# Kernel optimization log

Hardware: AMD Instinct MI355X
Metric: run time of the kernel (lower is better)

The kernel has to match this reference:

```python
import jax, jax.numpy as jnp
import numpy as np

WS = 7       # window_size
SHIFT = 3    # shift_size
HEADS = 3
EPS = 1e-5


def _rel_index():
    # (2, N) coords of a WS x WS window, then pairwise relative offsets -> flat table index
    coords = np.stack(np.meshgrid(np.arange(WS), np.arange(WS), indexing='ij')).reshape(2, -1)
    rel = (coords[:, :, None] - coords[:, None, :]).transpose(1, 2, 0) + (WS - 1)  # (N,N,2)
    return jnp.asarray(rel[..., 0] * (2 * WS - 1) + rel[..., 1])  # (N,N) int


def _layernorm(x, g, b):
    mu = jnp.mean(x, axis=-1, keepdims=True)
    var = jnp.mean(jnp.square(x - mu), axis=-1, keepdims=True)
    return (x - mu) * jax.lax.rsqrt(var + EPS) * g + b


def setup_inputs() -> dict:
    key = jax.random.key(0)
    ks = jax.random.split(key, 6)
    C, HID = 96, 384
    s = 0.02
    return {
        'x': jax.random.normal(ks[0], (8, C, 224, 224), jnp.float32),
        'norm1_g': jnp.ones((C,), jnp.float32),
        'norm1_b': jnp.zeros((C,), jnp.float32),
        'qkv_w': jax.random.normal(ks[1], (C, 3 * C), jnp.float32) * s,
        'qkv_b': jnp.zeros((3 * C,), jnp.float32),
        'proj_w': jax.random.normal(ks[2], (C, C), jnp.float32) * s,
        'proj_b': jnp.zeros((C,), jnp.float32),
        'rel_bias_table': jax.random.normal(ks[3], ((2 * WS - 1) ** 2, HEADS), jnp.float32) * s,
        'norm2_g': jnp.ones((C,), jnp.float32),
        'norm2_b': jnp.zeros((C,), jnp.float32),
        'fc1_w': jax.random.normal(ks[4], (C, HID), jnp.float32) * s,
        'fc1_b': jnp.zeros((HID,), jnp.float32),
        'fc2_w': jax.random.normal(ks[5], (HID, C), jnp.float32) * s,
        'fc2_b': jnp.zeros((C,), jnp.float32),
    }


def reference(x, norm1_g, norm1_b, qkv_w, qkv_b, proj_w, proj_b,
              rel_bias_table, norm2_g, norm2_b, fc1_w, fc1_b, fc2_w, fc2_b):
    B, C, H, W = x.shape
    N = WS * WS
    dh = C // HEADS

    # norm1 over channels (tokens = flattened spatial)
    xt = x.reshape(B, C, H * W).transpose(0, 2, 1)          # (B, L, C)
    xn = _layernorm(xt, norm1_g, norm1_b)
    xs = xn.transpose(0, 2, 1).reshape(B, C, H, W)
    # H, W divisible by WS -> pad is a no-op; cyclic shift
    xs = jnp.roll(xs, (-SHIFT, -SHIFT), axis=(2, 3))

    # window partition -> (B*nW, N, C)
    xw = xs.reshape(B, C, H // WS, WS, W // WS, WS)
    xw = xw.transpose(0, 2, 4, 3, 5, 1).reshape(-1, N, C)

    # window attention with relative position bias (no shift mask, per source)
    Bw = xw.shape[0]
    qkv = (xw @ qkv_w + qkv_b).reshape(Bw, N, 3, HEADS, dh).transpose(2, 0, 3, 1, 4)
    q, k, v = qkv[0], qkv[1], qkv[2]                        # (Bw, h, N, dh)
    attn = jnp.einsum('bhnd,bhmd->bhnm', q, k) * (dh ** -0.5)
    bias = rel_bias_table[_rel_index().reshape(-1)].reshape(N, N, HEADS).transpose(2, 0, 1)
    attn = jax.nn.softmax(attn + bias, axis=-1)
    out = jnp.einsum('bhnm,bhmd->bhnd', attn, v).transpose(0, 2, 1, 3).reshape(Bw, N, C)
    out = out @ proj_w + proj_b

    # window reverse + unshift
    xr = out.reshape(B, H // WS, W // WS, WS, WS, C)
    xr = xr.transpose(0, 5, 1, 3, 2, 4).reshape(B, C, H, W)
    xr = jnp.roll(xr, (SHIFT, SHIFT), axis=(2, 3))

    x = x + xr                                              # residual 1

    # MLP branch with norm2 (exact GELU, matching torch nn.GELU default)
    xt = x.reshape(B, C, H * W).transpose(0, 2, 1)
    xn = _layernorm(xt, norm2_g, norm2_b)
    h = jax.nn.gelu(xn @ fc1_w + fc1_b, approximate=False)
    h = h @ fc2_w + fc2_b
    return x + h.transpose(0, 2, 1).reshape(B, C, H, W)
```

## Files before the change

### kernel.cpp

```cpp
#include <hip/hip_runtime.h>
#include <hip/hip_bf16.h>
#include <math.h>

#define WSZ 7
#define NTOK 49
#define CH 96
#define HIMG 224
#define WIMG 224
#define HWIMG (224*224)
#define SHIFT_ 3
#define HID 384

typedef __attribute__((ext_vector_type(8))) short bf16x8;
typedef __attribute__((ext_vector_type(4))) float f32x4;
typedef unsigned int u32;
typedef unsigned short u16;

__device__ __forceinline__ u32 pk2(float a, float b) {
    u16 ua = __builtin_bit_cast(u16, __float2bfloat16(a));
    u16 ub = __builtin_bit_cast(u16, __float2bfloat16(b));
    return (u32)ua | ((u32)ub << 16);
}

union FragU { u32 w[4]; bf16x8 v; };

__device__ __forceinline__ bf16x8 regroup(u32 t0w0, u32 t0w1, u32 t1w0, u32 t1w1, int lane) {
    int sl0 = (lane & 15) + ((lane & 16) << 1);
    int sl1 = sl0 + 16;
    u32 x0 = (u32)__shfl((int)t0w0, sl0);
    u32 y0 = (u32)__shfl((int)t1w0, sl0);
    u32 x1 = (u32)__shfl((int)t0w1, sl0);
    u32 y1 = (u32)__shfl((int)t1w1, sl0);
    u32 x2 = (u32)__shfl((int)t0w0, sl1);
    u32 y2 = (u32)__shfl((int)t1w0, sl1);
    u32 x3 = (u32)__shfl((int)t0w1, sl1);
    u32 y3 = (u32)__shfl((int)t1w1, sl1);
    bool lo = lane < 32;
    FragU f;
    f.w[0] = lo ? x0 : y0;
    f.w[1] = lo ? x1 : y1;
    f.w[2] = lo ? x2 : y2;
    f.w[3] = lo ? x3 : y3;
    return f.v;
}

__device__ __forceinline__ float gelu_f(float x) {
    float x2 = x * x;
    float s  = x * (0.7978845608028654f + 0.03567740813636141f * x2);
    float e  = __expf(2.0f * s);
    float th = 1.0f - 2.0f / (e + 1.0f);
    return 0.5f * x * (1.0f + th);
}

__global__ __launch_bounds__(256) void prep_kernel(
    const float* __restrict__ w1, const float* __restrict__ w2,
    const float* __restrict__ pw, const float* __restrict__ qw,
    __hip_bfloat16* __restrict__ ws, int n)
{
    int i = blockIdx.x * 256 + threadIdx.x;
    if (i >= n) return;
    float val = 0.f;
    if (i < 81920) {
        int ch = i / 20480, r = i - ch * 20480;
        int half = r / 10240;
        int rr = r - half * 10240;
        if (rr < 9984) {
            int row = rr / 104, col = rr - row * 104;
            if (col < 96)
                val = (half == 0) ? w1[col * HID + ch * 96 + row]
                                  : w2[(size_t)(ch * 96 + col) * CH + row];
        }
    } else if (i < 92160) {
        int r = i - 81920;
        if (r < 9984) {
            int row = r / 104, col = r - row * 104;
            if (col < 96) val = pw[col * CH + row];
        }
    } else {
        int j = i - 92160;
        int hh = j / 9984, rr = j - hh * 9984;
        int dp = rr / 104, c = rr - dp * 104;
        if (c < 96) {
            int colW = (dp < 32) ? (hh * 32 + dp)
                     : (dp < 64) ? (96 + hh * 32 + dp - 32)
                                 : (192 + hh * 32 + dp - 64);
            val = qw[c * 288 + colW];
        }
    }
    ws[i] = __float2bfloat16(val);
}

__global__ __launch_bounds__(256) void attn2_kernel(
    const float* __restrict__ x,
    const float* __restrict__ g1, const float* __restrict__ b1,
    const __hip_bfloat16* __restrict__ wsW,
    const float* __restrict__ qkv_b, const float* __restrict__ pb,
    const float* __restrict__ btab,
    __hip_bfloat16* __restrict__ projout)
{
    const int tid  = threadIdx.x;
    const int lane = tid & 63;
    const int wv   = tid >> 6;
    const int l15  = lane & 15;
    const int g    = lane >> 4;
    const int bi   = blockIdx.x;
    const int b    = bi >> 8;
    const int wh   = (bi >> 3) & 31;
    const int ww0  = (bi & 7) * 4;
    const int ww   = ww0 + wv;

    __shared__ float btabL[507];
    __shared__ __align__(16) char uniA[43008];

    __hip_bfloat16 (*xsb)[7][32] = (__hip_bfloat16(*)[7][32])uniA;
    __hip_bfloat16 (*vT)[72] = (__hip_bfloat16(*)[72])(uniA + wv * 4608);
    u32* prS = (u32*)(uniA + wv * 4608);

    for (int idx = tid; idx < 507; idx += 256) btabL[idx] = btab[idx];

    const int colBase = ww0 * 7 + 3;
    const int cA  = colBase & ~3;
    const int cb4 = cA >> 2;
    const int a0  = colBase & 3;
    #pragma unroll
    for (int k = 0; k < 21; ++k) {
        int idx = tid + 256 * k;
        int c = idx / 56, rem = idx - c * 56;
        int r = rem >> 3, cf = rem & 7;
        int gr = wh * 7 + 3 + r; if (gr >= HIMG) gr -= HIMG;
        int g4 = cb4 + cf; if (g4 >= 56) g4 -= 56;
        float4 v = *(const float4*)(x + ((size_t)(b * CH + c) * HIMG + gr) * WIMG + g4 * 4);
        uint2 pk;
        pk.x = pk2(v.x, v.y);
        pk.y = pk2(v.z, v.w);
        *(uint2*)&xsb[c][r][cf * 4] = pk;
    }
    __syncthreads();

    bf16x8 xB[4][3];
    #pragma unroll
    for (int it = 0; it < 4; ++it) {
        int i = it * 16 + l15;
        bool real = i < NTOK;
        int yi = i / 7, xi = i - yi * 7;
        int sc = a0 + wv * 7 + xi;
        float raw[24];
        float s0 = 0.f, s1 = 0.f;
        #pragma unroll
        for (int ks = 0; ks < 3; ++ks)
            #pragma unroll
            for (int t = 0; t < 8; ++t) {
                int c = ks * 32 + g * 8 + t;
                float v = real ? __bfloat162float(xsb[c][yi][sc]) : 0.f;
                raw[ks * 8 + t] = v; s0 += v; s1 += v * v;
            }
        s0 += __shfl_xor(s0, 16); s0 += __shfl_xor(s0, 32);
        s1 += __shfl_xor(s1, 16); s1 += __shfl_xor(s1, 32);
        float mu = s0 * (1.0f / CH);
        float rstd = rsqrtf(s1 * (1.0f / CH) - mu * mu + 1e-5f);
        #pragma unroll
        for (int ks = 0; ks < 3; ++ks)
            #pragma unroll
            for (int t = 0; t < 8; ++t) {
                int c = ks * 32 + g * 8 + t;
                float xv = real ? ((raw[ks * 8 + t] - mu) * rstd * g1[c] + b1[c]) : 0.f;
                xB[it][ks][t] = (short)__builtin_bit_cast(u16, __float2bfloat16(xv));
            }
    }
    __syncthreads();

    const float scale = 0.17677669529663687f;
    bf16x8 aoB[3][4];

    for (int h = 0; h < 3; ++h) {
        const __hip_bfloat16* qkvTg = wsW + 92160 + h * 9984;

        float qb[2][4], kb[2][4], vb[2][4];
        #pragma unroll
        for (int dt = 0; dt < 2; ++dt)
            #pragma unroll
            for (int r = 0; r < 4; ++r) {
                int d = h * 32 + dt * 16 + g * 4 + r;
                qb[dt][r] = qkv_b[d];
                kb[dt][r] = qkv_b[96 + d];
                vb[dt][r] = qkv_b[192 + d];
            }

        u32 Qpk[2][4][2];
        #pragma unroll
        for (int dt = 0; dt < 2; ++dt) {
            const __hip_bfloat16* wr = qkvTg + (dt * 16 + l15) * 104 + g * 8;
            bf16x8 a0f = *(const bf16x8*)(wr);
            bf16x8 a1f = *(const bf16x8*)(wr + 32);
            bf16x8 a2f = *(const bf16x8*)(wr + 64);
            #pragma unroll
            for (int it = 0; it < 4; ++it) {
                f32x4 c4 = {0.f, 0.f, 0.f, 0.f};
                c4 = __builtin_amdgcn_mfma_f32_16x16x32_bf16(a0f, xB[it][0], c4, 0, 0, 0);
                c4 = __builtin_amdgcn_mfma_f32_16x16x32_bf16(a1f, xB[it][1], c4, 0, 0, 0);
                c4 = __builtin_amdgcn_mfma_f32_16x16x32_bf16(a2f, xB[it][2], c4, 0, 0, 0);
                Qpk[dt][it][0] = pk2(c4[0] + qb[dt][0], c4[1] + qb[dt][1]);
                Qpk[dt][it][1] = pk2(c4[2] + qb[dt][2], c4[3] + qb[dt][3]);
            }
        }
        bf16x8 QB[4];
        #pragma unroll
        for (int it = 0; it < 4; ++it)
            QB[it] = regroup(Qpk[0][it][0], Qpk[0][it][1], Qpk[1][it][0], Qpk[1][it][1], lane);

        u32 Kpk[2][4][2];
        #pragma unroll
        for (int dt = 0; dt < 2; ++dt) {
            const __hip_bfloat16* wr = qkvTg + (32 + dt * 16 + l15) * 104 + g * 8;
            bf16x8 a0f = *(const bf16x8*)(wr);
            bf16x8 a1f = *(const bf16x8*)(wr + 32);
            bf16x8 a2f = *(const bf16x8*)(wr + 64);
            #pragma unroll
            for (int it = 0; it < 4; ++it) {
                f32x4 c4 = {0.f, 0.f, 0.f, 0.f};
                c4 = __builtin_amdgcn_mfma_f32_16x16x32_bf16(a0f, xB[it][0], c4, 0, 0, 0);
                c4 = __builtin_amdgcn_mfma_f32_16x16x32_bf16(a1f, xB[it][1], c4, 0, 0, 0);
                c4 = __builtin_amdgcn_mfma_f32_16x16x32_bf16(a2f, xB[it][2], c4, 0, 0, 0);
                Kpk[dt][it][0] = pk2(c4[0] + kb[dt][0], c4[1] + kb[dt][1]);
                Kpk[dt][it][1] = pk2(c4[2] + kb[dt][2], c4[3] + kb[dt][3]);
            }
        }
        bf16x8 KA[4];
        #pragma unroll
        for (int it = 0; it < 4; ++it)
            KA[it] = regroup(Kpk[0][it][0], Kpk[0][it][1], Kpk[1][it][0], Kpk[1][it][1], lane);

        #pragma unroll
        for (int dt = 0; dt < 2; ++dt) {
            const __hip_bfloat16* wr = qkvTg + (64 + dt * 16 + l15) * 104 + g * 8;
            bf16x8 a0f = *(const bf16x8*)(wr);
            bf16x8 a1f = *(const bf16x8*)(wr + 32);
            bf16x8 a2f = *(const bf16x8*)(wr + 64);
            #pragma unroll
            for (int it = 0; it < 4; ++it) {
                f32x4 c4 = {0.f, 0.f, 0.f, 0.f};
                c4 = __builtin_amdgcn_mfma_f32_16x16x32_bf16(a0f, xB[it][0], c4, 0, 0, 0);
                c4 = __builtin_amdgcn_mfma_f32_16x16x32_bf16(a1f, xB[it][1], c4, 0, 0, 0);
                c4 = __builtin_amdgcn_mfma_f32_16x16x32_bf16(a2f, xB[it][2], c4, 0, 0, 0);
                #pragma unroll
                for (int r = 0; r < 4; ++r)
                    vT[dt * 16 + g * 4 + r][it * 16 + l15] = __float2bfloat16(c4[r] + vb[dt][r]);
            }
        }
        bf16x8 VBf[2][2];
        #pragma unroll
        for (int dt = 0; dt < 2; ++dt)
            #pragma unroll
            for (int ks = 0; ks < 2; ++ks)
                VBf[dt][ks] = *(const bf16x8*)&vT[dt * 16 + l15][ks * 32 + g * 8];

        #pragma unroll
        for (int it = 0; it < 4; ++it) {
            f32x4 SC[4];
            #pragma unroll
            for (int jt = 0; jt < 4; ++jt) {
                f32x4 z = {0.f, 0.f, 0.f, 0.f};
                SC[jt] = __builtin_amdgcn_mfma_f32_16x16x32_bf16(KA[jt], QB[it], z, 0, 0, 0);
            }
            int i = it * 16 + l15;
            int yi = i / 7, xi = i - yi * 7;
            float p[16];
            float m = -1e30f;
            #pragma unroll
            for (int jt = 0; jt < 4; ++jt)
                #pragma unroll
                for (int r = 0; r < 4; ++r) {
                    int j = jt * 16 + g * 4 + r;
                    int yj = j / 7, xj = j - yj * 7;
                    int rel = (yi - yj + 6) * 13 + (xi - xj + 6);
                    rel = rel < 0 ? 0 : (rel > 168 ? 168 : rel);
                    float s = (j < NTOK) ? (SC[jt][r] * scale + btabL[rel * 3 + h]) : -1e30f;
                    p[jt * 4 + r] = s;
                    m = fmaxf(m, s);
                }
            m = fmaxf(m, __shfl_xor(m, 16));
            m = fmaxf(m, __shfl_xor(m, 32));
            float sum = 0.f;
            #pragma unroll
            for (int q = 0; q < 16; ++q) { float e = __expf(p[q] - m); p[q] = e; sum += e; }
            sum += __shfl_xor(sum, 16);
            sum += __shfl_xor(sum, 32);
            float inv = 1.f / sum;
            u32 Ppk[4][2];
            #pragma unroll
            for (int jt = 0; jt < 4; ++jt) {
                Ppk[jt][0] = pk2(p[jt * 4 + 0] * inv, p[jt * 4 + 1] * inv);
                Ppk[jt][1] = pk2(p[jt * 4 + 2] * inv, p[jt * 4 + 3] * inv);
            }
            bf16x8 PA0 = regroup(Ppk[0][0], Ppk[0][1], Ppk[1][0], Ppk[1][1], lane);
            bf16x8 PA1 = regroup(Ppk[2][0], Ppk[2][1], Ppk[3][0], Ppk[3][1], lane);
            u32 opk[2][2];
            #pragma unroll
            for (int dt = 0; dt < 2; ++dt) {
                f32x4 o = {0.f, 0.f, 0.f, 0.f};
                o = __builtin_amdgcn_mfma_f32_16x16x32_bf16(PA0, VBf[dt][0], o, 0, 0, 0);
                o = __builtin_amdgcn_mfma_f32_16x16x32_bf16(PA1, VBf[dt][1], o, 0, 0, 0);
                opk[dt][0] = pk2(o[0], o[1]);
                opk[dt][1] = pk2(o[2], o[3]);
            }
            aoB[h][it] = regroup(opk[0][0], opk[0][1], opk[1][0], opk[1][1], lane);
        }
    }

    const __hip_bfloat16* pwTg = wsW + 81920;
    for (int it = 0; it < 4; ++it) {
        #pragma unroll
        for (int mt = 0; mt < 6; ++mt) {
            const __hip_bfloat16* wr = pwTg + (mt * 16 + l15) * 104 + g * 8;
            f32x4 cp = {0.f, 0.f, 0.f, 0.f};
            #pragma unroll
            for (int ks = 0; ks < 3; ++ks) {
                bf16x8 af = *(const bf16x8*)(wr + ks * 32);
                cp = __builtin_amdgcn_mfma_f32_16x16x32_bf16(af, aoB[ks][it], cp, 0, 0, 0);
            }
            float v0 = cp[0] + pb[mt * 16 + g * 4 + 0];
            float v1 = cp[1] + pb[mt * 16 + g * 4 + 1];
            float v2 = cp[2] + pb[mt * 16 + g * 4 + 2];
            float v3 = cp[3] + pb[mt * 16 + g * 4 + 3];
            prS[l15 * 52 + mt * 8 + g * 2 + 0] = pk2(v0, v1);
            prS[l15 * 52 + mt * 8 + g * 2 + 1] = pk2(v2, v3);
        }
        #pragma unroll
        for (int s = 0; s < 3; ++s) {
            int chunk = lane + 64 * s;
            int row = chunk / 12, q = chunk - row * 12;
            int tok = it * 16 + row;
            if (tok < NTOK) {
                int yi = tok / 7, xi = tok - yi * 7;
                int hh = wh * 7 + yi + SHIFT_; if (hh >= HIMG) hh -= HIMG;
                int wp = ww * 7 + xi + SHIFT_; if (wp >= WIMG) wp -= WIMG;
                float4 val = *(const float4*)((const char*)prS + row * 208 + q * 16);
                *(float4*)(projout + ((size_t)b * HWIMG + hh * WIMG + wp) * 96 + q * 8) = val;
            }
        }
    }
}

__global__ __launch_bounds__(512, 4) void mlp2_kernel(
    const float* __restrict__ x, const __hip_bfloat16* __restrict__ projout,
    const float* __restrict__ g2, const float* __restrict__ b2,
    const float* __restrict__ bb1, const float* __restrict__ bb2,
    const __hip_bfloat16* __restrict__ wsW,
    float* __restrict__ out)
{
    const int tid = threadIdx.x;
    const int lane = tid & 63, wv = tid >> 6;
    const int l15 = lane & 15, g = lane >> 4;
    const int b = blockIdx.x / 392;
    const int hw0 = (blockIdx.x % 392) * 128;
    const int m0 = wv * 16;
    const int t = tid & 127;
    const int c0 = tid >> 7;

    __shared__ __align__(16) char WREG[46592];
    __shared__ __align__(16) __hip_bfloat16 xnS[128][104];
    __shared__ float part0[4][128], part1[4][128];
    __shared__ float muS[128], rsS[128];
    __shared__ float bb1S[HID];

    __hip_bfloat16 (*w1T)[104]  = (__hip_bfloat16(*)[104])WREG;
    __hip_bfloat16 (*w2T)[104]  = (__hip_bfloat16(*)[104])(WREG + 20480);
    __hip_bfloat16 (*obuf)[104] = (__hip_bfloat16(*)[104])WREG;

    float xreg[24];

    for (int idx = tid, k = 0; idx < 96 * 128; idx += 512, ++k) {
        int c = idx >> 7, tt = idx & 127;
        xreg[k] = x[(size_t)(b * CH + c) * HWIMG + hw0 + tt];
    }
    #pragma unroll
    for (int s = 0; s < 3; ++s) {
        int chunk = tid + 512 * s;
        int row = chunk / 12, q = chunk - row * 12;
        *(float4*)&xnS[row][q * 8] =
            *(const float4*)(projout + ((size_t)b * HWIMG + hw0 + row) * 96 + q * 8);
    }
    for (int idx = tid; idx < HID; idx += 512) bb1S[idx] = bb1[idx];
    __syncthreads();

    {
        float s0 = 0.f, s1 = 0.f;
        #pragma unroll
        for (int k = 0; k < 24; ++k) {
            int c = c0 + 4 * k;
            float v = xreg[k] + __bfloat162float(xnS[t][c]);
            xreg[k] = v; s0 += v; s1 += v * v;
        }
        part0[c0][t] = s0; part1[c0][t] = s1;
    }
    __syncthreads();
    if (tid < 128) {
        float s0 = part0[0][tid] + part0[1][tid] + part0[2][tid] + part0[3][tid];
        float s1 = part1[0][tid] + part1[1][tid] + part1[2][tid] + part1[3][tid];
        float m = s0 * (1.0f / CH);
        muS[tid] = m;
        rsS[tid] = rsqrtf(s1 * (1.0f / CH) - m * m + 1e-5f);
    }
    __syncthreads();
    #pragma unroll
    for (int k = 0; k < 24; ++k) {
        int c = c0 + 4 * k;
        xnS[t][c] = __float2bfloat16((xreg[k] - muS[t]) * rsS[t] * g2[c] + b2[c]);
    }
    __syncthreads();

    bf16x8 xbf[3];
    #pragma unroll
    for (int ks = 0; ks < 3; ++ks)
        xbf[ks] = *(const bf16x8*)&xnS[m0 + l15][ks * 32 + g * 8];

    f32x4 acc[6];
    #pragma unroll
    for (int mt = 0; mt < 6; ++mt)
        #pragma unroll
        for (int r = 0; r < 4; ++r)
            acc[mt][r] = bb2[mt * 16 + g * 4 + r];

    for (int ch = 0; ch < 4; ++ch) {
        {
            const float4* src = (const float4*)wsW + (size_t)ch * 2560;
            float4* dst = (float4*)WREG;
            #pragma unroll
            for (int i = tid; i < 2560; i += 512) dst[i] = src[i];
        }
        __syncthreads();

        u32 hpk[6][2];
        #pragma unroll
        for (int mt = 0; mt < 6; ++mt) {
            f32x4 f = {0.f, 0.f, 0.f, 0.f};
            #pragma unroll
            for (int ks = 0; ks < 3; ++ks) {
                bf16x8 af = *(const bf16x8*)&w1T[mt * 16 + l15][ks * 32 + g * 8];
                f = __builtin_amdgcn_mfma_f32_16x16x32_bf16(af, xbf[ks], f, 0, 0, 0);
            }
            float gl[4];
            #pragma unroll
            for (int r = 0; r < 4; ++r) {
                float a = f[r] + bb1S[ch * 96 + mt * 16 + g * 4 + r];
                gl[r] = gelu_f(a);
            }
            hpk[mt][0] = pk2(gl[0], gl[1]);
            hpk[mt][1] = pk2(gl[2], gl[3]);
        }
        bf16x8 hf[3];
        hf[0] = regroup(hpk[0][0], hpk[0][1], hpk[1][0], hpk[1][1], lane);
        hf[1] = regroup(hpk[2][0], hpk[2][1], hpk[3][0], hpk[3][1], lane);
        hf[2] = regroup(hpk[4][0], hpk[4][1], hpk[5][0], hpk[5][1], lane);

        #pragma unroll
        for (int mt = 0; mt < 6; ++mt) {
            #pragma unroll
            for (int ks = 0; ks < 3; ++ks) {
                bf16x8 af = *(const bf16x8*)&w2T[mt * 16 + l15][ks * 32 + g * 8];
                acc[mt] = __builtin_amdgcn_mfma_f32_16x16x32_bf16(af, hf[ks], acc[mt], 0, 0, 0);
            }
        }
        __syncthreads();
    }

    #pragma unroll
    for (int mt = 0; mt < 6; ++mt)
        #pragma unroll
        for (int r = 0; r < 4; ++r)
            obuf[m0 + l15][mt * 16 + g * 4 + r] = __float2bfloat16(acc[mt][r]);
    __syncthreads();
    #pragma unroll
    for (int k = 0; k < 24; ++k) {
        int c = c0 + 4 * k;
        out[(size_t)(b * CH + c) * HWIMG + hw0 + t] = xreg[k] + __bfloat162float(obuf[t][c]);
    }
}

__global__ __launch_bounds__(256) void attn_mfma_kernel(
    const float* __restrict__ x,
    const float* __restrict__ g1, const float* __restrict__ b1,
    const float* __restrict__ qkv_w, const float* __restrict__ qkv_b,
    const float* __restrict__ btab,
    float* __restrict__ ao)
{
    const int tid  = threadIdx.x;
    const int lane = tid & 63;
    const int wv   = tid >> 6;
    const int l15  = lane & 15;
    const int g    = lane >> 4;
    const int wid  = blockIdx.x * 4 + wv;
    const int b    = wid >> 10;
    const int wh   = (wid >> 5) & 31;
    const int ww   = wid & 31;

    __shared__ __align__(16) __hip_bfloat16 wT[96][104];
    __shared__ float btabL[507];
    __shared__ __align__(16) __hip_bfloat16 vT[4][32][72];
    __shared__ __align__(16) __hip_bfloat16 Ob[4][64][36];

    int to_h = 0, to_w = 0;
    if (lane < NTOK) {
        int yl = lane / 7, xl = lane - yl * 7;
        to_h = wh * 7 + yl + SHIFT_; if (to_h >= HIMG) to_h -= HIMG;
        to_w = ww * 7 + xl + SHIFT_; if (to_w >= WIMG) to_w -= WIMG;
    }

    bf16x8 xB[4][3];
    #pragma unroll
    for (int it = 0; it < 4; ++it) {
        int i = it * 16 + l15;
        bool real = i < NTOK;
        int yi = i / 7, xi = i - yi * 7;
        int hh = wh * 7 + yi + SHIFT_; if (hh >= HIMG) hh -= HIMG;
        int wp = ww * 7 + xi + SHIFT_; if (wp >= WIMG) wp -= WIMG;
        float raw[24];
        float s0 = 0.f, s1 = 0.f;
        #pragma unroll
        for (int ks = 0; ks < 3; ++ks)
            #pragma unroll
            for (int t = 0; t < 8; ++t) {
                int c = ks * 32 + g * 8 + t;
                float v = real ? x[((size_t)(b * CH + c) * HIMG + hh) * WIMG + wp] : 0.f;
                raw[ks * 8 + t] = v; s0 += v; s1 += v * v;
            }
        s0 += __shfl_xor(s0, 16); s0 += __shfl_xor(s0, 32);
        s1 += __shfl_xor(s1, 16); s1 += __shfl_xor(s1, 32);
        float mu = s0 * (1.0f / CH);
        float rstd = rsqrtf(s1 * (1.0f / CH) - mu * mu + 1e-5f);
        #pragma unroll
        for (int ks = 0; ks < 3; ++ks)
            #pragma unroll
            for (int t = 0; t < 8; ++t) {
                int c = ks * 32 + g * 8 + t;
                float xv = real ? ((raw[ks * 8 + t] - mu) * rstd * g1[c] + b1[c]) : 0.f;
                xB[it][ks][t] = (short)__builtin_bit_cast(u16, __float2bfloat16(xv));
            }
    }

    const float scale = 0.17677669529663687f;

    for (int h = 0; h < 3; ++h) {
        __syncthreads();
        for (int idx = tid; idx < 96 * 96; idx += 256) {
            int c = idx / 96, dp = idx - c * 96;
            int col = (dp < 32) ? (h * 32 + dp) : (dp < 64) ? (96 + h * 32 + dp - 32)
                                                            : (192 + h * 32 + dp - 64);
            wT[dp][c] = __float2bfloat16(qkv_w[c * 288 + col]);
        }
        if (h == 0)
            for (int idx = tid; idx < 507; idx += 256) btabL[idx] = btab[idx];
        __syncthreads();

        float qb[2][4], kb[2][4], vb[2][4];
        #pragma unroll
        for (int dt = 0; dt < 2; ++dt)
            #pragma unroll
            for (int r = 0; r < 4; ++r) {
                int d = h * 32 + dt * 16 + g * 4 + r;
                qb[dt][r] = qkv_b[d];
                kb[dt][r] = qkv_b[96 + d];
                vb[dt][r] = qkv_b[192 + d];
            }

        u32 Qpk[2][4][2];
        #pragma unroll
        for (int dt = 0; dt < 2; ++dt) {
            bf16x8 a0 = *(const bf16x8*)&wT[dt * 16 + l15][0 * 32 + g * 8];
            bf16x8 a1 = *(const bf16x8*)&wT[dt * 16 + l15][1 * 32 + g * 8];
            bf16x8 a2 = *(const bf16x8*)&wT[dt * 16 + l15][2 * 32 + g * 8];
            #pragma unroll
            for (int it = 0; it < 4; ++it) {
                f32x4 c4 = {0.f, 0.f, 0.f, 0.f};
                c4 = __builtin_amdgcn_mfma_f32_16x16x32_bf16(a0, xB[it][0], c4, 0, 0, 0);
                c4 = __builtin_amdgcn_mfma_f32_16x16x32_bf16(a1, xB[it][1], c4, 0, 0, 0);
                c4 = __builtin_amdgcn_mfma_f32_16x16x32_bf16(a2, xB[it][2], c4, 0, 0, 0);
                Qpk[dt][it][0] = pk2(c4[0] + qb[dt][0], c4[1] + qb[dt][1]);
                Qpk[dt][it][1] = pk2(c4[2] + qb[dt][2], c4[3] + qb[dt][3]);
            }
        }
        bf16x8 QB[4];
        #pragma unroll
        for (int it = 0; it < 4; ++it)
            QB[it] = regroup(Qpk[0][it][0], Qpk[0][it][1], Qpk[1][it][0], Qpk[1][it][1], lane);

        u32 Kpk[2][4][2];
        #pragma unroll
        for (int dt = 0; dt < 2; ++dt) {
            bf16x8 a0 = *(const bf16x8*)&wT[32 + dt * 16 + l15][0 * 32 + g * 8];
            bf16x8 a1 = *(const bf16x8*)&wT[32 + dt * 16 + l15][1 * 32 + g * 8];
            bf16x8 a2 = *(const bf16x8*)&wT[32 + dt * 16 + l15][2 * 32 + g * 8];
            #pragma unroll
            for (int it = 0; it < 4; ++it) {
                f32x4 c4 = {0.f, 0.f, 0.f, 0.f};
                c4 = __builtin_amdgcn_mfma_f32_16x16x32_bf16(a0, xB[it][0], c4, 0, 0, 0);
                c4 = __builtin_amdgcn_mfma_f32_16x16x32_bf16(a1, xB[it][1], c4, 0, 0, 0);
                c4 = __builtin_amdgcn_mfma_f32_16x16x32_bf16(a2, xB[it][2], c4, 0, 0, 0);
                Kpk[dt][it][0] = pk2(c4[0] + kb[dt][0], c4[1] + kb[dt][1]);
                Kpk[dt][it][1] = pk2(c4[2] + kb[dt][2], c4[3] + kb[dt][3]);
            }
        }
        bf16x8 KA[4];
        #pragma unroll
        for (int it = 0; it < 4; ++it)
            KA[it] = regroup(Kpk[0][it][0], Kpk[0][it][1], Kpk[1][it][0], Kpk[1][it][1], lane);

        #pragma unroll
        for (int dt = 0; dt < 2; ++dt) {
            bf16x8 a0 = *(const bf16x8*)&wT[64 + dt * 16 + l15][0 * 32 + g * 8];
            bf16x8 a1 = *(const bf16x8*)&wT[64 + dt * 16 + l15][1 * 32 + g * 8];
            bf16x8 a2 = *(const bf16x8*)&wT[64 + dt * 16 + l15][2 * 32 + g * 8];
            #pragma unroll
            for (int it = 0; it < 4; ++it) {
                f32x4 c4 = {0.f, 0.f, 0.f, 0.f};
                c4 = __builtin_amdgcn_mfma_f32_16x16x32_bf16(a0, xB[it][0], c4, 0, 0, 0);
                c4 = __builtin_amdgcn_mfma_f32_16x16x32_bf16(a1, xB[it][1], c4, 0, 0, 0);
                c4 = __builtin_amdgcn_mfma_f32_16x16x32_bf16(a2, xB[it][2], c4, 0, 0, 0);
                #pragma unroll
                for (int r = 0; r < 4; ++r)
                    vT[wv][dt * 16 + g * 4 + r][it * 16 + l15] = __float2bfloat16(c4[r] + vb[dt][r]);
            }
        }
        bf16x8 VBf[2][2];
        #pragma unroll
        for (int dt = 0; dt < 2; ++dt)
            #pragma unroll
            for (int ks = 0; ks < 2; ++ks)
                VBf[dt][ks] = *(const bf16x8*)&vT[wv][dt * 16 + l15][ks * 32 + g * 8];

        #pragma unroll
        for (int it = 0; it < 4; ++it) {
            f32x4 SC[4];
            #pragma unroll
            for (int jt = 0; jt < 4; ++jt) {
                f32x4 z = {0.f, 0.f, 0.f, 0.f};
                SC[jt] = __builtin_amdgcn_mfma_f32_16x16x32_bf16(KA[jt], QB[it], z, 0, 0, 0);
            }
            int i = it * 16 + l15;
            int yi = i / 7, xi = i - yi * 7;
            float p[16];
            float m = -1e30f;
            #pragma unroll
            for (int jt = 0; jt < 4; ++jt)
                #pragma unroll
                for (int r = 0; r < 4; ++r) {
                    int j = jt * 16 + g * 4 + r;
                    int yj = j / 7, xj = j - yj * 7;
                    int rel = (yi - yj + 6) * 13 + (xi - xj + 6);
                    rel = rel < 0 ? 0 : (rel > 168 ? 168 : rel);
                    float s = (j < NTOK) ? (SC[jt][r] * scale + btabL[rel * 3 + h]) : -1e30f;
                    p[jt * 4 + r] = s;
                    m = fmaxf(m, s);
                }
            m = fmaxf(m, __shfl_xor(m, 16));
            m = fmaxf(m, __shfl_xor(m, 32));
            float sum = 0.f;
            #pragma unroll
            for (int q = 0; q < 16; ++q) { float e = __expf(p[q] - m); p[q] = e; sum += e; }
            sum += __shfl_xor(sum, 16);
            sum += __shfl_xor(sum, 32);
            float inv = 1.f / sum;
            u32 Ppk[4][2];
            #pragma unroll
            for (int jt = 0; jt < 4; ++jt) {
                Ppk[jt][0] = pk2(p[jt * 4 + 0] * inv, p[jt * 4 + 1] * inv);
                Ppk[jt][1] = pk2(p[jt * 4 + 2] * inv, p[jt * 4 + 3] * inv);
            }
            bf16x8 PA0 = regroup(Ppk[0][0], Ppk[0][1], Ppk[1][0], Ppk[1][1], lane);
            bf16x8 PA1 = regroup(Ppk[2][0], Ppk[2][1], Ppk[3][0], Ppk[3][1], lane);
            #pragma unroll
            for (int dt = 0; dt < 2; ++dt) {
                f32x4 o = {0.f, 0.f, 0.f, 0.f};
                o = __builtin_amdgcn_mfma_f32_16x16x32_bf16(PA0, VBf[dt][0], o, 0, 0, 0);
                o = __builtin_amdgcn_mfma_f32_16x16x32_bf16(PA1, VBf[dt][1], o, 0, 0, 0);
                #pragma unroll
                for (int r = 0; r < 4; ++r)
                    Ob[wv][it * 16 + g * 4 + r][dt * 16 + l15] = __float2bfloat16(o[r]);
            }
        }

        if (lane < NTOK) {
            #pragma unroll 8
            for (int ch = 0; ch < 32; ++ch)
                ao[((size_t)(b * CH + h * 32 + ch) * HIMG + to_h) * WIMG + to_w] =
                    __bfloat162float(Ob[wv][lane][ch]);
        }
    }
}

__global__ __launch_bounds__(512, 4) void fuse2_kernel(
    const float* __restrict__ x, const float* ao,
    const float* __restrict__ pw, const float* __restrict__ pb,
    const float* __restrict__ g2, const float* __restrict__ b2,
    const float* __restrict__ w1, const float* __restrict__ bb1,
    const float* __restrict__ w2, const float* __restrict__ bb2,
    const __hip_bfloat16* __restrict__ wsW, int useWs,
    float* out)
{
    const int tid = threadIdx.x;
    const int lane = tid & 63, wv = tid >> 6;
    const int l15 = lane & 15, g = lane >> 4;
    const int b = blockIdx.x / 392;
    const int hw0 = (blockIdx.x % 392) * 128;
    const int m0 = wv * 16;
    const int t = tid & 127;
    const int c0 = tid >> 7;

    __shared__ __align__(16) char WREG[46592];
    __shared__ __align__(16) __hip_bfloat16 xnS[128][104];
    __shared__ float part0[4][128], part1[4][128];
    __shared__ float muS[128], rsS[128];
    __shared__ float bb1S[HID];

    __hip_bfloat16 (*pwT)[104]   = (__hip_bfloat16(*)[104])WREG;
    __hip_bfloat16 (*projS)[104] = (__hip_bfloat16(*)[104])(WREG + 19968);
    __hip_bfloat16 (*w1T)[104]   = (__hip_bfloat16(*)[104])WREG;
    __hip_bfloat16 (*w2T)[104]   = (__hip_bfloat16(*)[104])(WREG + 20480);
    __hip_bfloat16 (*obuf)[104]  = (__hip_bfloat16(*)[104])WREG;

    float xreg[24];

    for (int idx = tid, k = 0; idx < 96 * 128; idx += 512, ++k) {
        int c = idx >> 7, tt = idx & 127;
        size_t gi = (size_t)(b * CH + c) * HWIMG + hw0 + tt;
        xreg[k] = x[gi];
        xnS[tt][c] = __float2bfloat16(ao[gi]);
    }
    if (useWs) {
        const float4* src = (const float4*)wsW + 10240;
        float4* dst = (float4*)WREG;
        for (int i = tid; i < 1280; i += 512) dst[i] = src[i];
    } else {
        for (int idx = tid; idx < 96 * 96; idx += 512) {
            int c = idx / 96, oc = idx - c * 96;
            pwT[oc][c] = __float2bfloat16(pw[c * 96 + oc]);
        }
    }
    for (int idx = tid; idx < HID; idx += 512) bb1S[idx] = bb1[idx];
    __syncthreads();

    {
        bf16x8 bfr[3];
        #pragma unroll
        for (int ks = 0; ks < 3; ++ks)
            bfr[ks] = *(const bf16x8*)&xnS[m0 + l15][ks * 32 + g * 8];
        #pragma unroll
        for (int mt = 0; mt < 6; ++mt) {
            f32x4 cp = {0.f, 0.f, 0.f, 0.f};
            #pragma unroll
            for (int ks = 0; ks < 3; ++ks) {
                bf16x8 af = *(const bf16x8*)&pwT[mt * 16 + l15][ks * 32 + g * 8];
                cp = __builtin_amdgcn_mfma_f32_16x16x32_bf16(af, bfr[ks], cp, 0, 0, 0);
            }
            #pragma unroll
            for (int r = 0; r < 4; ++r) {
                int oc = mt * 16 + g * 4 + r;
                projS[m0 + l15][oc] = __float2bfloat16(cp[r] + pb[oc]);
            }
        }
    }
    __syncthreads();

    {
        float s0 = 0.f, s1 = 0.f;
        #pragma unroll
        for (int k = 0; k < 24; ++k) {
            int c = c0 + 4 * k;
            float v = xreg[k] + __bfloat162float(projS[t][c]);
            xreg[k] = v; s0 += v; s1 += v * v;
        }
        part0[c0][t] = s0; part1[c0][t] = s1;
    }
    __syncthreads();
    if (tid < 128) {
        float s0 = part0[0][tid] + part0[1][tid] + part0[2][tid] + part0[3][tid];
        float s1 = part1[0][tid] + part1[1][tid] + part1[2][tid] + part1[3][tid];
        float m = s0 * (1.0f / CH);
        muS[tid] = m;
        rsS[tid] = rsqrtf(s1 * (1.0f / CH) - m * m + 1e-5f);
    }
    __syncthreads();
    #pragma unroll
    for (int k = 0; k < 24; ++k) {
        int c = c0 + 4 * k;
        xnS[t][c] = __float2bfloat16((xreg[k] - muS[t]) * rsS[t] * g2[c] + b2[c]);
    }
    __syncthreads();

    bf16x8 xbf[3];
    #pragma unroll
    for (int ks = 0; ks < 3; ++ks)
        xbf[ks] = *(const bf16x8*)&xnS[m0 + l15][ks * 32 + g * 8];

    f32x4 acc[6];
    #pragma unroll
    for (int mt = 0; mt < 6; ++mt)
        #pragma unroll
        for (int r = 0; r < 4; ++r)
            acc[mt][r] = bb2[mt * 16 + g * 4 + r];

    for (int ch = 0; ch < 4; ++ch) {
        if (useWs) {
            const float4* src = (const float4*)wsW + (size_t)ch * 2560;
            float4* dst = (float4*)WREG;
            #pragma unroll
            for (int i = tid; i < 2560; i += 512) dst[i] = src[i];
        } else {
            for (int idx = tid; idx < 2 * 96 * 96; idx += 512) {
                if (idx < 9216) {
                    int kk = idx / 96, n = idx - kk * 96;
                    w1T[n][kk] = __float2bfloat16(w1[kk * HID + ch * 96 + n]);
                } else {
                    int j = idx - 9216;
                    int kk = j / 96, n = j - kk * 96;
                    w2T[n][kk] = __float2bfloat16(w2[(size_t)(ch * 96 + kk) * CH + n]);
                }
            }
        }
        __syncthreads();

        u32 hpk[6][2];
        #pragma unroll
        for (int mt = 0; mt < 6; ++mt) {
            f32x4 f = {0.f, 0.f, 0.f, 0.f};
            #pragma unroll
            for (int ks = 0; ks < 3; ++ks) {
                bf16x8 af = *(const bf16x8*)&w1T[mt * 16 + l15][ks * 32 + g * 8];
                f = __builtin_amdgcn_mfma_f32_16x16x32_bf16(af, xbf[ks], f, 0, 0, 0);
            }
            float gl[4];
            #pragma unroll
            for (int r = 0; r < 4; ++r) {
                float a = f[r] + bb1S[ch * 96 + mt * 16 + g * 4 + r];
                gl[r] = gelu_f(a);
            }
            hpk[mt][0] = pk2(gl[0], gl[1]);
            hpk[mt][1] = pk2(gl[2], gl[3]);
        }
        bf16x8 hf[3];
        hf[0] = regroup(hpk[0][0], hpk[0][1], hpk[1][0], hpk[1][1], lane);
        hf[1] = regroup(hpk[2][0], hpk[2][1], hpk[3][0], hpk[3][1], lane);
        hf[2] = regroup(hpk[4][0], hpk[4][1], hpk[5][0], hpk[5][1], lane);

        #pragma unroll
        for (int mt = 0; mt < 6; ++mt)
            #pragma unroll
            for (int ks = 0; ks < 3; ++ks) {
                bf16x8 af = *(const bf16x8*)&w2T[mt * 16 + l15][ks * 32 + g * 8];
                acc[mt] = __builtin_amdgcn_mfma_f32_16x16x32_bf16(af, hf[ks], acc[mt], 0, 0, 0);
            }
        __syncthreads();
    }

    #pragma unroll
    for (int mt = 0; mt < 6; ++mt)
        #pragma unroll
        for (int r = 0; r < 4; ++r)
            obuf[m0 + l15][mt * 16 + g * 4 + r] = __float2bfloat16(acc[mt][r]);
    __syncthreads();
    #pragma unroll
    for (int k = 0; k < 24; ++k) {
        int c = c0 + 4 * k;
        out[(size_t)(b * CH + c) * HWIMG + hw0 + t] = xreg[k] + __bfloat162float(obuf[t][c]);
    }
}

extern "C" void kernel_launch(void* const* d_in, const int* in_sizes, int n_in,
                              void* d_out, int out_size, void* d_ws, size_t ws_size,
                              hipStream_t stream) {
    const float* x    = (const float*)d_in[0];
    const float* n1g  = (const float*)d_in[1];
    const float* n1b  = (const float*)d_in[2];
    const float* qkvw = (const float*)d_in[3];
    const float* qkvb = (const float*)d_in[4];
    const float* pw   = (const float*)d_in[5];
    const float* pbv  = (const float*)d_in[6];
    const float* bt   = (const float*)d_in[7];
    const float* n2g  = (const float*)d_in[8];
    const float* n2b  = (const float*)d_in[9];
    const float* f1w  = (const float*)d_in[10];
    const float* f1b  = (const float*)d_in[11];
    const float* f2w  = (const float*)d_in[12];
    const float* f2b  = (const float*)d_in[13];
    float* out = (float*)d_out;

    const size_t FULL_NEED = 262144ull + 77070336ull;
    if (ws_size >= FULL_NEED) {
        __hip_bfloat16* wsW = (__hip_bfloat16*)d_ws;
        __hip_bfloat16* projout = (__hip_bfloat16*)((char*)d_ws + 262144);
        prep_kernel<<<477, 256, 0, stream>>>(f1w, f2w, pw, qkvw, wsW, 122112);
        attn2_kernel<<<2048, 256, 0, stream>>>(x, n1g, n1b, wsW, qkvb, pbv, bt, projout);
        mlp2_kernel<<<3136, 512, 0, stream>>>(x, projout, n2g, n2b, f1b, f2b, wsW, out);
    } else {
        int useWs = (ws_size >= 184320) ? 1 : 0;
        if (useWs)
            prep_kernel<<<360, 256, 0, stream>>>(f1w, f2w, pw, qkvw, (__hip_bfloat16*)d_ws, 92160);
        attn_mfma_kernel<<<2048, 256, 0, stream>>>(x, n1g, n1b, qkvw, qkvb, bt, out);
        fuse2_kernel<<<3136, 512, 0, stream>>>(x, out, pw, pbv, n2g, n2b, f1w, f1b, f2w, f2b,
                                               (const __hip_bfloat16*)d_ws, useWs, out);
    }
}
```

Baseline: 455.4 us.

## Shrink MLP kernel LDS via per-wave LayerNorm and single weight buffer

The MLP kernel now computes residual-add and LayerNorm per token inside each wave using MFMA fragment layout and cross-lane shuffles, which removes the partial-sum shared arrays and several block barriers. Weight staging now uses one half-size LDS buffer that is reloaded between fc1 and fc2 for each hidden chunk, so shared memory drops from about 74KB to about 28KB, allowing more blocks per CU. In exchange it adds two extra barriers and a second global weight load per chunk. The global reads and writes of x become strided per lane rather than coalesced across tokens.

```diff
diff --git a/kernel.cpp b/kernel.cpp
--- a/kernel.cpp
+++ b/kernel.cpp
@@ -21,6 +21,7 @@
     u16 ub = __builtin_bit_cast(u16, __float2bfloat16(b));
     return (u32)ua | ((u32)ub << 16);
 }
+__device__ __forceinline__ float bflo(u32 u) { return __builtin_bit_cast(float, u << 16); }
 
 union FragU { u32 w[4]; bf16x8 v; };
 
@@ -353,26 +354,15 @@
     const int l15 = lane & 15, g = lane >> 4;
     const int b = blockIdx.x / 392;
     const int hw0 = (blockIdx.x % 392) * 128;
-    const int m0 = wv * 16;
-    const int t = tid & 127;
-    const int c0 = tid >> 7;
-
-    __shared__ __align__(16) char WREG[46592];
-    __shared__ __align__(16) __hip_bfloat16 xnS[128][104];
-    __shared__ float part0[4][128], part1[4][128];
-    __shared__ float muS[128], rsS[128];
+    const int tok = wv * 16 + l15;
+
+    __shared__ __align__(16) char SB[26624];
     __shared__ float bb1S[HID];
 
-    __hip_bfloat16 (*w1T)[104]  = (__hip_bfloat16(*)[104])WREG;
-    __hip_bfloat16 (*w2T)[104]  = (__hip_bfloat16(*)[104])(WREG + 20480);
-    __hip_bfloat16 (*obuf)[104] = (__hip_bfloat16(*)[104])WREG;
-
-    float xreg[24];
-
-    for (int idx = tid, k = 0; idx < 96 * 128; idx += 512, ++k) {
-        int c = idx >> 7, tt = idx & 127;
-        xreg[k] = x[(size_t)(b * CH + c) * HWIMG + hw0 + tt];
-    }
+    __hip_bfloat16 (*xnS)[104]  = (__hip_bfloat16(*)[104])SB;
+    __hip_bfloat16 (*wT)[104]   = (__hip_bfloat16(*)[104])SB;
+    __hip_bfloat16 (*obuf)[104] = (__hip_bfloat16(*)[104])SB;
+
     #pragma unroll
     for (int s = 0; s < 3; ++s) {
         int chunk = tid + 512 * s;
@@ -383,50 +373,55 @@
     for (int idx = tid; idx < HID; idx += 512) bb1S[idx] = bb1[idx];
     __syncthreads();
 
-    {
-        float s0 = 0.f, s1 = 0.f;
-        #pragma unroll
-        for (int k = 0; k < 24; ++k) {
-            int c = c0 + 4 * k;
-            float v = xreg[k] + __bfloat162float(xnS[t][c]);
-            xreg[k] = v; s0 += v; s1 += v * v;
-        }
-        part0[c0][t] = s0; part1[c0][t] = s1;
-    }
-    __syncthreads();
-    if (tid < 128) {
-        float s0 = part0[0][tid] + part0[1][tid] + part0[2][tid] + part0[3][tid];
-        float s1 = part1[0][tid] + part1[1][tid] + part1[2][tid] + part1[3][tid];
-        float m = s0 * (1.0f / CH);
-        muS[tid] = m;
-        rsS[tid] = rsqrtf(s1 * (1.0f / CH) - m * m + 1e-5f);
-    }
-    __syncthreads();
-    #pragma unroll
-    for (int k = 0; k < 24; ++k) {
-        int c = c0 + 4 * k;
-        xnS[t][c] = __float2bfloat16((xreg[k] - muS[t]) * rsS[t] * g2[c] + b2[c]);
-    }
-    __syncthreads();
+    float xr[24];
+    float s0 = 0.f, s1 = 0.f;
+    bf16x8 pf[3];
+    #pragma unroll
+    for (int ks = 0; ks < 3; ++ks)
+        pf[ks] = *(const bf16x8*)&xnS[tok][ks * 32 + g * 8];
+    const float* xb = x + (size_t)(b * CH) * HWIMG + hw0 + tok;
+    #pragma unroll
+    for (int ks = 0; ks < 3; ++ks)
+        #pragma unroll
+        for (int j = 0; j < 8; ++j) {
+            int c = ks * 32 + g * 8 + j;
+            float xv = xb[(size_t)c * HWIMG];
+            float v = xv + bflo((u32)(u16)pf[ks][j]);
+            xr[ks * 8 + j] = v; s0 += v; s1 += v * v;
+        }
+    s0 += __shfl_xor(s0, 16); s0 += __shfl_xor(s0, 32);
+    s1 += __shfl_xor(s1, 16); s1 += __shfl_xor(s1, 32);
+    float mu = s0 * (1.0f / CH);
+    float rstd = rsqrtf(s1 * (1.0f / CH) - mu * mu + 1e-5f);
 
     bf16x8 xbf[3];
     #pragma unroll
-    for (int ks = 0; ks < 3; ++ks)
-        xbf[ks] = *(const bf16x8*)&xnS[m0 + l15][ks * 32 + g * 8];
+    for (int ks = 0; ks < 3; ++ks) {
+        float nv[8];
+        #pragma unroll
+        for (int j = 0; j < 8; ++j) {
+            int c = ks * 32 + g * 8 + j;
+            nv[j] = (xr[ks * 8 + j] - mu) * rstd * g2[c] + b2[c];
+        }
+        FragU f;
+        f.w[0] = pk2(nv[0], nv[1]); f.w[1] = pk2(nv[2], nv[3]);
+        f.w[2] = pk2(nv[4], nv[5]); f.w[3] = pk2(nv[6], nv[7]);
+        xbf[ks] = f.v;
+    }
+    __syncthreads();
 
     f32x4 acc[6];
     #pragma unroll
-    for (int mt = 0; mt < 6; ++mt)
-        #pragma unroll
-        for (int r = 0; r < 4; ++r)
-            acc[mt][r] = bb2[mt * 16 + g * 4 + r];
+    for (int mt = 0; mt < 6; ++mt) {
+        #pragma unroll
+        for (int r = 0; r < 4; ++r) acc[mt][r] = bb2[mt * 16 + g * 4 + r];
+    }
 
     for (int ch = 0; ch < 4; ++ch) {
         {
             const float4* src = (const float4*)wsW + (size_t)ch * 2560;
-            float4* dst = (float4*)WREG;
-            #pragma unroll
-            for (int i = tid; i < 2560; i += 512) dst[i] = src[i];
+            #pragma unroll
+            for (int i = tid; i < 1280; i += 512) ((float4*)SB)[i] = src[i];
         }
         __syncthreads();
 
@@ -436,7 +431,7 @@
             f32x4 f = {0.f, 0.f, 0.f, 0.f};
             #pragma unroll
             for (int ks = 0; ks < 3; ++ks) {
-                bf16x8 af = *(const bf16x8*)&w1T[mt * 16 + l15][ks * 32 + g * 8];
+                bf16x8 af = *(const bf16x8*)&wT[mt * 16 + l15][ks * 32 + g * 8];
                 f = __builtin_amdgcn_mfma_f32_16x16x32_bf16(af, xbf[ks], f, 0, 0, 0);
             }
             float gl[4];
@@ -448,6 +443,15 @@
             hpk[mt][0] = pk2(gl[0], gl[1]);
             hpk[mt][1] = pk2(gl[2], gl[3]);
         }
+        __syncthreads();
+
+        {
+            const float4* src = (const float4*)wsW + (size_t)ch * 2560 + 1280;
+            #pragma unroll
+            for (int i = tid; i < 1280; i += 512) ((float4*)SB)[i] = src[i];
+        }
+        __syncthreads();
+
         bf16x8 hf[3];
         hf[0] = regroup(hpk[0][0], hpk[0][1], hpk[1][0], hpk[1][1], lane);
         hf[1] = regroup(hpk[2][0], hpk[2][1], hpk[3][0], hpk[3][1], lane);
@@ -457,7 +461,7 @@
         for (int mt = 0; mt < 6; ++mt) {
             #pragma unroll
             for (int ks = 0; ks < 3; ++ks) {
-                bf16x8 af = *(const bf16x8*)&w2T[mt * 16 + l15][ks * 32 + g * 8];
+                bf16x8 af = *(const bf16x8*)&wT[mt * 16 + l15][ks * 32 + g * 8];
                 acc[mt] = __builtin_amdgcn_mfma_f32_16x16x32_bf16(af, hf[ks], acc[mt], 0, 0, 0);
             }
         }
@@ -468,12 +472,17 @@
     for (int mt = 0; mt < 6; ++mt)
         #pragma unroll
         for (int r = 0; r < 4; ++r)
-            obuf[m0 + l15][mt * 16 + g * 4 + r] = __float2bfloat16(acc[mt][r]);
-    __syncthreads();
-    #pragma unroll
-    for (int k = 0; k < 24; ++k) {
-        int c = c0 + 4 * k;
-        out[(size_t)(b * CH + c) * HWIMG + hw0 + t] = xreg[k] + __bfloat162float(obuf[t][c]);
+            obuf[tok][mt * 16 + g * 4 + r] = __float2bfloat16(acc[mt][r]);
+    __syncthreads();
+    #pragma unroll
+    for (int ks = 0; ks < 3; ++ks) {
+        bf16x8 ov = *(const bf16x8*)&obuf[tok][ks * 32 + g * 8];
+        #pragma unroll
+        for (int j = 0; j < 8; ++j) {
+            int c = ks * 32 + g * 8 + j;
+            out[(size_t)(b * CH + c) * HWIMG + hw0 + tok] =
+                xr[ks * 8 + j] + bflo((u32)(u16)ov[j]);
+        }
     }
 }
 
```

Result: no change. 458.2 us (+0.6%).
